# Optimization experiments

Hardware: AMD Instinct MI355X
Metric: run time of the kernel (lower is better)

Reference implementation:

```python
import jax, jax.numpy as jnp
import numpy as np

H = 40; W = 40; WS = 8; SHIFT = 4; NH = 10; C = 60; HD = C // NH
N = WS * WS; NW = (H // WS) * (W // WS); NB = 4; EPS = 1e-5

def _rel_pos_index():
    coords = np.stack(np.meshgrid(np.arange(WS), np.arange(WS), indexing='ij')).reshape(2, -1)
    rel = (coords[:, :, None] - coords[:, None, :]).transpose(1, 2, 0)
    rel[:, :, 0] += WS - 1; rel[:, :, 1] += WS - 1; rel[:, :, 0] *= 2 * WS - 1
    return jnp.asarray(rel.sum(-1))  # [N, N]

RPI = _rel_pos_index()

def _shift_mask():
    img = np.zeros((H, W))
    cnt = 0
    sls = (slice(0, -WS), slice(-WS, -SHIFT), slice(-SHIFT, None))
    for hs in sls:
        for ws_ in sls:
            img[hs, ws_] = cnt; cnt += 1
    mw = img.reshape(H // WS, WS, W // WS, WS).transpose(0, 2, 1, 3).reshape(NW, N)
    am = mw[:, None, :] - mw[:, :, None]
    return jnp.asarray(np.where(am != 0, -100.0, 0.0).astype(np.float32))  # [NW, N, N]

MASK = _shift_mask()

def _ln(x, g, b):
    m = x.mean(-1, keepdims=True)
    v = ((x - m) ** 2).mean(-1, keepdims=True)
    return (x - m) * jax.lax.rsqrt(v + EPS) * g + b

def _win_part(x):  # [B,H,W,C] -> [B*NW,N,C]
    B = x.shape[0]
    return x.reshape(B, H // WS, WS, W // WS, WS, C).transpose(0, 1, 3, 2, 4, 5).reshape(B * NW, N, C)

def _win_rev(x, B):  # [B*NW,N,C] -> [B,H,W,C]
    return x.reshape(B, H // WS, W // WS, WS, WS, C).transpose(0, 1, 3, 2, 4, 5).reshape(B, H, W, C)

def _block(x, p, shift):
    B = x.shape[0]
    g1, b1, qkvw, qkvb, rpb_t, pw, pb, g2, b2, f1w, f1b, f2w, f2b = p
    shortcut = x
    h = _ln(x, g1, b1).reshape(B, H, W, C)
    if shift:
        h = jnp.roll(h, (-shift, -shift), axis=(1, 2))
    xw = _win_part(h)                                   # [B*NW, N, C]
    qkv = (xw @ qkvw.T + qkvb).reshape(-1, N, 3, NH, HD).transpose(2, 0, 3, 1, 4)
    q, k, v = qkv[0], qkv[1], qkv[2]                    # [B*NW, NH, N, HD]
    attn = (q * (HD ** -0.5)) @ k.transpose(0, 1, 3, 2)  # [B*NW, NH, N, N]
    attn = attn + rpb_t[RPI].transpose(2, 0, 1)[None]
    if shift:
        attn = (attn.reshape(B, NW, NH, N, N) + MASK[None, :, None]).reshape(-1, NH, N, N)
    attn = jax.nn.softmax(attn, axis=-1)
    o = (attn @ v).transpose(0, 2, 1, 3).reshape(-1, N, C)
    o = o @ pw.T + pb
    h = _win_rev(o, B)
    if shift:
        h = jnp.roll(h, (shift, shift), axis=(1, 2))
    x = shortcut + h.reshape(B, H * W, C)
    y = _ln(x, g2, b2)
    y = jax.nn.gelu(y @ f1w.T + f1b, approximate=False) @ f2w.T + f2b
    return x + y

def _conv(x, w, b):
    y = jax.lax.conv_general_dilated(x, w, (1, 1), 'SAME', dimension_numbers=('NCHW', 'OIHW', 'NCHW'))
    return y + b[None, :, None, None]

def _forward(x, conv_in_w, conv_in_b, norm1_g, norm1_b, qkv_w, qkv_b, rpb, proj_w, proj_b,
             norm2_g, norm2_b, fc1_w, fc1_b, fc2_w, fc2_b, conv_out_w, conv_out_b):
    B = x.shape[0]
    h = _conv(x.reshape(B, -1, H, W), conv_in_w, conv_in_b)   # [B, C, H, W]
    h = h.reshape(B, C, H * W).transpose(0, 2, 1)             # [B, L, C]
    for i in range(NB):
        p = (norm1_g[i], norm1_b[i], qkv_w[i], qkv_b[i], rpb[i], proj_w[i], proj_b[i],
             norm2_g[i], norm2_b[i], fc1_w[i], fc1_b[i], fc2_w[i], fc2_b[i])
        h = _block(h, p, SHIFT if i % 2 == 1 else 0)
    h = h.transpose(0, 2, 1).reshape(B, C, H, W)
    return _conv(h, conv_out_w, conv_out_b)


def setup_inputs() -> dict:
    key = jax.random.key(0)
    ks = jax.random.split(key, 10)
    s = 0.02
    return {
        'x': jax.random.normal(ks[0], (128, 6, 3, H, W), jnp.float32),
        'conv_in_w': jax.random.normal(ks[1], (C, 18, 3, 3), jnp.float32) * s,
        'conv_in_b': jnp.zeros((C,), jnp.float32),
        'norm1_g': jnp.ones((NB, C), jnp.float32),
        'norm1_b': jnp.zeros((NB, C), jnp.float32),
        'qkv_w': jax.random.normal(ks[2], (NB, 3 * C, C), jnp.float32) * s,
        'qkv_b': jnp.zeros((NB, 3 * C), jnp.float32),
        'rpb': jax.random.normal(ks[3], (NB, (2 * WS - 1) ** 2, NH), jnp.float32) * s,
        'proj_w': jax.random.normal(ks[4], (NB, C, C), jnp.float32) * s,
        'proj_b': jnp.zeros((NB, C), jnp.float32),
        'norm2_g': jnp.ones((NB, C), jnp.float32),
        'norm2_b': jnp.zeros((NB, C), jnp.float32),
        'fc1_w': jax.random.normal(ks[5], (NB, 4 * C, C), jnp.float32) * s,
        'fc1_b': jnp.zeros((NB, 4 * C), jnp.float32),
        'fc2_w': jax.random.normal(ks[6], (NB, C, 4 * C), jnp.float32) * s,
        'fc2_b': jnp.zeros((NB, C), jnp.float32),
        'conv_out_w': jax.random.normal(ks[7], (3, C, 3, 3), jnp.float32) * s,
        'conv_out_b': jnp.zeros((3,), jnp.float32),
    }


def reference(x, conv_in_w, conv_in_b, norm1_g, norm1_b, qkv_w, qkv_b, rpb, proj_w, proj_b,
              norm2_g, norm2_b, fc1_w, fc1_b, fc2_w, fc2_b, conv_out_w, conv_out_b):
    return _forward(x, conv_in_w, conv_in_b, norm1_g, norm1_b, qkv_w, qkv_b, rpb, proj_w, proj_b,
                    norm2_g, norm2_b, fc1_w, fc1_b, fc2_w, fc2_b, conv_out_w, conv_out_b)
```

## Files before the change

### kernel.cpp

```cpp
#include <hip/hip_runtime.h>
#include <math.h>


typedef __bf16 bf16x8 __attribute__((ext_vector_type(8)));
typedef float f32x4 __attribute__((ext_vector_type(4)));
typedef unsigned int u32x4 __attribute__((ext_vector_type(4)));
typedef float f4u __attribute__((ext_vector_type(4), aligned(4)));

#define MFMA16(a, b, c) __builtin_amdgcn_mfma_f32_16x16x32_bf16(a, b, c, 0, 0, 0)

__device__ __forceinline__ unsigned short f2bf(float x) {
    unsigned u = __float_as_uint(x);
    return (unsigned short)((u + 0x7fffu + ((u >> 16) & 1u)) >> 16);
}
__device__ __forceinline__ unsigned short bfrn(float x) {
    return (unsigned short)((__float_as_uint(x) + 0x8000u) >> 16);
}
__device__ __forceinline__ unsigned pk2rn(float a, float b) {
    unsigned r;
    asm("v_cvt_pk_bf16_f32 %0, %1, %2" : "=v"(r) : "v"(a), "v"(b));
    return r;
}
__device__ __forceinline__ float bfsel(unsigned u, int hi) {
    return __uint_as_float(hi ? (u & 0xffff0000u) : (u << 16));
}
__device__ __forceinline__ float gelu_f(float v) {
    float t2 = v * v;
    float e = __builtin_amdgcn_exp2f(v * fmaf(0.102943225f, t2, 2.302207877f));
    float r = __builtin_amdgcn_rcpf(e + 1.f);
    return fmaf(-v, r, v);
}
__device__ __forceinline__ int gidx(int n, int wh, int wc, int shift) {
    int hh = wh * 8 + (n >> 3) + shift; if (hh >= 40) hh -= 40;
    int ww = wc * 8 + (n & 7) + shift;  if (ww >= 40) ww -= 40;
    return hh * 40 + ww;
}

__global__ __launch_bounds__(256) void prep_k(
    const float* __restrict__ qkvw, const float* __restrict__ pw,
    const float* __restrict__ f1w, const float* __restrict__ f2w,
    const float* __restrict__ qkvb, const float* __restrict__ pb,
    const float* __restrict__ f1b, const float* __restrict__ f2b,
    const float* __restrict__ g1v, const float* __restrict__ b1v,
    const float* __restrict__ g2v, const float* __restrict__ b2v,
    unsigned short* __restrict__ Wp)
{
    int t = blockIdx.x * 256 + threadIdx.x;
    int lane = t & 63;
    int q6 = t >> 6;
    int layer = q6 / 96, tile = q6 % 96;
    int l15 = lane & 15, l4 = lane >> 4;
    const float* src; const float* gam = 0; const float* bet = 0;
    float bias = 0.f, rowscale = 1.f;
    int row, stride, rmax, kmax, k0;
    unsigned short* dst = Wp + layer * 49152;
    if (tile < 24) {
        int ot = tile >> 1, ks = tile & 1;
        src = qkvw + layer * 10800; row = ot * 16 + l15; k0 = ks * 32 + l4 * 8;
        rmax = 180; kmax = 60; stride = 60; dst += tile * 512;
        gam = g1v + layer * 60; bet = b1v + layer * 60;
        if (row < 180) bias = qkvb[layer * 180 + row];
        if (row < 60) rowscale = 0.58897780f;
    } else if (tile < 32) {
        int tt = tile - 24;
        src = pw + layer * 3600; row = (tt >> 1) * 16 + l15; k0 = (tt & 1) * 32 + l4 * 8;
        rmax = 60; kmax = 60; stride = 60; dst += 12288 + tt * 512;
        if (row < 60) bias = pb[layer * 60 + row];
    } else if (tile < 64) {
        int tt = tile - 32; int ks = tt & 1; int po = tt >> 1; int ot = po & 7; int ph = po >> 3;
        src = f1w + layer * 14400 + ph * 7200; row = ot * 16 + l15; k0 = ks * 32 + l4 * 8;
        rmax = 120; kmax = 60; stride = 60; dst += 16384 + tt * 512;
        gam = g2v + layer * 60; bet = b2v + layer * 60;
        if (row < 120) bias = f1b[layer * 240 + ph * 120 + row];
    } else {
        int tt = tile - 64; int ks = tt & 3; int po = tt >> 2; int ot = po & 3; int ph = po >> 2;
        src = f2w + layer * 14400 + ph * 120; row = ot * 16 + l15; k0 = ks * 32 + l4 * 8;
        rmax = 60; kmax = 120; stride = 240; dst += 32768 + tt * 512;
        if (ph == 0 && row < 60) bias = f2b[layer * 60 + row];
    }
    unsigned short v[8];
    #pragma unroll
    for (int i = 0; i < 8; i++) {
        int k = k0 + i;
        float f = 0.f;
        if (row < rmax) {
            if (k < kmax) {
                f = src[row * stride + k];
                if (gam) f *= gam[k];
            } else if (k == kmax) {
                f = bias;
                if (bet) for (int kk = 0; kk < kmax; kk++) f += src[row * stride + kk] * bet[kk];
            }
        }
        v[i] = f2bf(f * rowscale);
    }
    unsigned a0 = (unsigned)v[0] | ((unsigned)v[1] << 16);
    unsigned a1 = (unsigned)v[2] | ((unsigned)v[3] << 16);
    unsigned a2 = (unsigned)v[4] | ((unsigned)v[5] << 16);
    unsigned a3 = (unsigned)v[6] | ((unsigned)v[7] << 16);
    *(uint4*)(dst + lane * 8) = make_uint4(a0, a1, a2, a3);
}

__global__ __launch_bounds__(256) void prepc_k(
    const float* __restrict__ ciw, const float* __restrict__ cow,
    unsigned short* __restrict__ Wc)
{
    int t = blockIdx.x * 256 + threadIdx.x;
    if (t >= 3456) return;
    int lane = t & 63, tile = t >> 6;
    int l15 = lane & 15, l4 = lane >> 4;
    unsigned short v[8];
    if (tile < 36) {
        int mt = tile / 9, g = tile % 9;
        int ky = g / 3, kx = g % 3;
        int row = mt * 16 + l15;
        int ci0 = l4 * 8;
        #pragma unroll
        for (int i = 0; i < 8; i++) {
            int ci = ci0 + i;
            float f = (row < 60 && ci < 18) ? ciw[(row * 18 + ci) * 9 + ky * 3 + kx] : 0.f;
            v[i] = f2bf(f);
        }
    } else {
        int tt = tile - 36;
        int g = tt >> 1, ks = tt & 1;
        int row = l15;
        int ci0 = ks * 32 + l4 * 8;
        #pragma unroll
        for (int i = 0; i < 8; i++) {
            int ci = ci0 + i;
            float f = (row < 3 && ci < 60) ? cow[(row * 60 + ci) * 9 + g] : 0.f;
            v[i] = f2bf(f);
        }
    }
    unsigned a0 = (unsigned)v[0] | ((unsigned)v[1] << 16);
    unsigned a1 = (unsigned)v[2] | ((unsigned)v[3] << 16);
    unsigned a2 = (unsigned)v[4] | ((unsigned)v[5] << 16);
    unsigned a3 = (unsigned)v[6] | ((unsigned)v[7] << 16);
    *(uint4*)(Wc + tile * 512 + lane * 8) = make_uint4(a0, a1, a2, a3);
}

__global__ __launch_bounds__(256) void rpbexp_k(
    const float* __restrict__ rpb, unsigned* __restrict__ rpbE)
{
    int layer = blockIdx.x / 5, hp = blockIdx.x % 5;
    int tid = threadIdx.x;
    int q = tid >> 2, j0 = (tid & 3) * 16;
    const float* rsrc = rpb + layer * 2250 + hp * 2;
    unsigned* dst = rpbE + ((layer * 5 + hp) * 64 + q) * 64 + j0;
    int qr = q >> 3, qc = q & 7;
    #pragma unroll
    for (int jj = 0; jj < 16; jj++) {
        int j = j0 + jj;
        int jr = j >> 3, jc = j & 7;
        int ridx = ((qr - jr + 7) * 15 + (qc - jc + 7)) * 10;
        unsigned short lo = f2bf(rsrc[ridx] * 1.4426950409f);
        unsigned short hi = f2bf(rsrc[ridx + 1] * 1.4426950409f);
        dst[jj] = (unsigned)lo | ((unsigned)hi << 16);
    }
}

__global__ __launch_bounds__(256) void conv_in_k(
    const float* __restrict__ x, const unsigned short* __restrict__ Wc,
    const float* __restrict__ bias, float* __restrict__ S)
{
    __shared__ __align__(16) unsigned short xt[10 * 42 * 32];
    int b = blockIdx.x / 5, y0 = (blockIdx.x % 5) * 8;
    int tid = threadIdx.x;
    int lane = tid & 63, w = tid >> 6;
    int l15 = lane & 15, l4 = lane >> 4;

    uint4* xt4 = (uint4*)xt;
    for (int i = tid; i < 1680; i += 256) xt4[i] = make_uint4(0u, 0u, 0u, 0u);
    __syncthreads();

    const float* xb = x + (size_t)b * 28800;
    for (int idx = tid; idx < 10 * 18 * 40; idx += 256) {
        int xx = idx % 40;
        int rem = idx / 40;
        int ci = rem % 18;
        int ry = rem / 18;
        int yy = y0 + ry - 1;
        if (yy >= 0 && yy < 40) {
            float v = xb[ci * 1600 + yy * 40 + xx];
            int xs = xx + 1;
            int bo = (((ry * 42 + xs) * 32 + ci) * 2) ^ ((xs & 3) << 4);
            *(unsigned short*)((char*)xt + bo) = bfrn(v);
        }
    }
    __syncthreads();

    bf16x8 afr[9];
    #pragma unroll
    for (int g = 0; g < 9; g++)
        afr[g] = *(const bf16x8*)(Wc + (w * 9 + g) * 512 + lane * 8);

    int c0 = w * 16 + l4 * 4;
    bool valid = (c0 < 60);
    f4u bv = {0.f, 0.f, 0.f, 0.f};
    if (valid) bv = *(const f4u*)(bias + c0);
    const f32x4 zf = {0.f, 0.f, 0.f, 0.f};
    const char* xtb = (const char*)xt;

    for (int nt = 0; nt < 20; nt++) {
        int tok = nt * 16 + l15;
        int yl = tok / 40, xl = tok % 40;
        f32x4 acc = zf;
        #pragma unroll
        for (int g = 0; g < 9; g++) {
            int ky = g / 3, kx = g % 3;
            int xs = xl + kx;
            int ba = ((yl + ky) * 42 + xs) * 64 + ((l4 ^ (xs & 3)) << 4);
            bf16x8 bfrag = *(const bf16x8*)(xtb + ba);
            acc = MFMA16(afr[g], bfrag, acc);
        }
        if (valid) {
            float4 r;
            r.x = acc[0] + bv[0]; r.y = acc[1] + bv[1];
            r.z = acc[2] + bv[2]; r.w = acc[3] + bv[3];
            *(float4*)(S + ((size_t)b * 1600 + y0 * 40 + tok) * 60 + c0) = r;
        }
    }
}

template<int SHIFT>
__global__ __launch_bounds__(256, 3) void block_k(
    float* __restrict__ S,
    const unsigned short* __restrict__ WpL,
    const unsigned* __restrict__ rpE)
{
    __shared__ __align__(16) unsigned char LDSA[53616];
    unsigned short* Pl  = (unsigned short*)(LDSA + 4608);
    float*          x1t = (float*)(LDSA + 0);
    unsigned short* xln = (unsigned short*)(LDSA + 15600);
    unsigned short* h1  = (unsigned short*)(LDSA + 15600);
    unsigned short* qn  = (unsigned short*)(LDSA + 24816);
    unsigned short* kn  = (unsigned short*)(LDSA + 34032);
    unsigned short* vt  = (unsigned short*)(LDSA + 43248);
    unsigned short* ln2 = (unsigned short*)(LDSA + 43248);

    const int tid = threadIdx.x;
    const int lane = tid & 63, w = tid >> 6;
    const int l15 = lane & 15, l4 = lane >> 4;
    const int wbase = w * 16;
    const int b = blockIdx.x / 25, wnd = blockIdx.x % 25;
    const int wh = wnd / 5, wc = wnd % 5;
    float* Sb = S + (size_t)b * 96000;
    const f32x4 zf = {0.f, 0.f, 0.f, 0.f};
    u32x4 zu = {0u, 0u, 0u, 0u};
    const bf16x8 zb = __builtin_bit_cast(bf16x8, zu);
    u32x4 ou = {0x3F803F80u, 0x3F803F80u, 0x3F803F80u, 0x3F803F80u};
    const bf16x8 ones = __builtin_bit_cast(bf16x8, ou);

    {
        int n = tid >> 2, p = tid & 3, cb = p * 16;
        int g = gidx(n, wh, wc, SHIFT);
        const float* xp = Sb + (size_t)g * 60 + cb;
        float xv[16];
        {
            float4 v0 = *(const float4*)xp;
            float4 v1 = *(const float4*)(xp + 4);
            float4 v2 = *(const float4*)(xp + 8);
            xv[0] = v0.x; xv[1] = v0.y; xv[2] = v0.z; xv[3] = v0.w;
            xv[4] = v1.x; xv[5] = v1.y; xv[6] = v1.z; xv[7] = v1.w;
            xv[8] = v2.x; xv[9] = v2.y; xv[10] = v2.z; xv[11] = v2.w;
            if (p < 3) {
                float4 v3 = *(const float4*)(xp + 12);
                xv[12] = v3.x; xv[13] = v3.y; xv[14] = v3.z; xv[15] = v3.w;
            } else { xv[12] = xv[13] = xv[14] = xv[15] = 0.f; }
        }
        float s = 0.f;
        #pragma unroll
        for (int ii = 0; ii < 16; ii++) s += xv[ii];
        s += __shfl_xor(s, 1); s += __shfl_xor(s, 2);
        float mean = s * (1.f / 60.f);
        float vv = 0.f;
        #pragma unroll
        for (int ii = 0; ii < 12; ii++) { float d = xv[ii] - mean; vv += d * d; }
        #pragma unroll
        for (int ii = 12; ii < 16; ii++) { float d = xv[ii] - mean; vv += (p < 3) ? d * d : 0.f; }
        vv += __shfl_xor(vv, 1); vv += __shfl_xor(vv, 2);
        float rs = rsqrtf(vv * (1.f / 60.f) + 1e-5f);
        float ov[16];
        #pragma unroll
        for (int ii = 0; ii < 12; ii++) ov[ii] = (xv[ii] - mean) * rs;
        #pragma unroll
        for (int ii = 12; ii < 16; ii++)
            ov[ii] = (p < 3) ? (xv[ii] - mean) * rs : ((ii == 12) ? 1.f : 0.f);
        unsigned short* xr = xln + n * 72 + cb;
        *(uint4*)xr = make_uint4(pk2rn(ov[0], ov[1]), pk2rn(ov[2], ov[3]),
                                 pk2rn(ov[4], ov[5]), pk2rn(ov[6], ov[7]));
        *(uint4*)(xr + 8) = make_uint4(pk2rn(ov[8], ov[9]), pk2rn(ov[10], ov[11]),
                                       pk2rn(ov[12], ov[13]), pk2rn(ov[14], ov[15]));
    }
    __syncthreads();

    {
        bf16x8 bx[4][2];
        #pragma unroll
        for (int nt = 0; nt < 4; nt++)
            #pragma unroll
            for (int ks = 0; ks < 2; ks++)
                bx[nt][ks] = *(const bf16x8*)(xln + (nt * 16 + l15) * 72 + l4 * 8 + ks * 32);
        #pragma unroll
        for (int t = 0; t < 3; t++) {
            int ot = w * 3 + t;
            f32x4 acc[4];
            #pragma unroll
            for (int nt = 0; nt < 4; nt++) acc[nt] = zf;
            #pragma unroll
            for (int ks = 0; ks < 2; ks++) {
                bf16x8 a = *(const bf16x8*)(WpL + (ot * 2 + ks) * 512 + lane * 8);
                #pragma unroll
                for (int nt = 0; nt < 4; nt++) acc[nt] = MFMA16(a, bx[nt][ks], acc[nt]);
            }
            int o0 = ot * 16 + l4 * 4;
            #pragma unroll
            for (int nt = 0; nt < 4; nt++) {
                int n = nt * 16 + l15;
                if (o0 < 60) {
                    *(uint2*)(qn + n * 72 + o0) =
                        make_uint2(pk2rn(acc[nt][0], acc[nt][1]), pk2rn(acc[nt][2], acc[nt][3]));
                } else if (o0 < 120) {
                    *(uint2*)(kn + n * 72 + (o0 - 60)) =
                        make_uint2(pk2rn(acc[nt][0], acc[nt][1]), pk2rn(acc[nt][2], acc[nt][3]));
                } else {
                    int r = o0 - 120;
                    vt[(r + 0) * 72 + n] = bfrn(acc[nt][0]);
                    vt[(r + 1) * 72 + n] = bfrn(acc[nt][1]);
                    vt[(r + 2) * 72 + n] = bfrn(acc[nt][2]);
                    vt[(r + 3) * 72 + n] = bfrn(acc[nt][3]);
                }
            }
        }
    }
    __syncthreads();

    unsigned maskbits = 0u;
    if (SHIFT) {
        int qtok = wbase + l15;
        int qr = qtok >> 3, qc = qtok & 7;
        int shp = wh * 8 + qr, swp = wc * 8 + qc;
        int qreg = (shp < 32 ? 0 : (shp < 36 ? 1 : 2)) * 3 + (swp < 32 ? 0 : (swp < 36 ? 1 : 2));
        #pragma unroll
        for (int e = 0; e < 16; e++) {
            int jt = e >> 2, r = e & 3;
            int j = jt * 16 + l4 * 4 + r;
            int jr = j >> 3, jc = j & 7;
            int shq = wh * 8 + jr, swq = wc * 8 + jc;
            int jreg = (shq < 32 ? 0 : (shq < 36 ? 1 : 2)) * 3 + (swq < 32 ? 0 : (swq < 36 ? 1 : 2));
            if (jreg != qreg) maskbits |= (1u << e);
        }
    }

    f32x4 oacc[10];
    #pragma unroll
    for (int h = 0; h < 10; h++) oacc[h] = zf;
    unsigned short* prow = Pl + (wbase + l15) * 72;
    const unsigned* rpq = rpE + ((wbase + l15) << 6) + (l4 << 2);

    u32x4 rpc[4];
    #pragma unroll
    for (int jt = 0; jt < 4; jt++) rpc[jt] = *(const u32x4*)(rpq + jt * 16);

    #pragma unroll
    for (int hp = 0; hp < 5; hp++) {
        u32x4 rpn[4];
        if (hp < 4) {
            const unsigned* rq = rpq + (hp + 1) * 4096;
            #pragma unroll
            for (int jt = 0; jt < 4; jt++) rpn[jt] = *(const u32x4*)(rq + jt * 16);
        }
        #pragma unroll
        for (int hh2 = 0; hh2 < 2; hh2++) {
            const int h = hp * 2 + hh2;
            bf16x8 bq = zb, ak0 = zb, ak1 = zb, ak2 = zb, ak3 = zb;
            if (l4 == 0) {
                const unsigned* qp = (const unsigned*)(qn + (wbase + l15) * 72 + h * 6);
                u32x4 uq = {qp[0], qp[1], qp[2], 0u};
                bq = __builtin_bit_cast(bf16x8, uq);
                const unsigned* k0p = (const unsigned*)(kn + (0 * 16 + l15) * 72 + h * 6);
                const unsigned* k1p = (const unsigned*)(kn + (1 * 16 + l15) * 72 + h * 6);
                const unsigned* k2p = (const unsigned*)(kn + (2 * 16 + l15) * 72 + h * 6);
                const unsigned* k3p = (const unsigned*)(kn + (3 * 16 + l15) * 72 + h * 6);
                u32x4 u0 = {k0p[0], k0p[1], k0p[2], 0u}; ak0 = __builtin_bit_cast(bf16x8, u0);
                u32x4 u1 = {k1p[0], k1p[1], k1p[2], 0u}; ak1 = __builtin_bit_cast(bf16x8, u1);
                u32x4 u2 = {k2p[0], k2p[1], k2p[2], 0u}; ak2 = __builtin_bit_cast(bf16x8, u2);
                u32x4 u3 = {k3p[0], k3p[1], k3p[2], 0u}; ak3 = __builtin_bit_cast(bf16x8, u3);
            }
            f32x4 s0 = MFMA16(ak0, bq, zf);
            f32x4 s1 = MFMA16(ak1, bq, zf);
            f32x4 s2 = MFMA16(ak2, bq, zf);
            f32x4 s3 = MFMA16(ak3, bq, zf);
            float ee[16];
            #pragma unroll
            for (int r = 0; r < 4; r++) {
                ee[0 + r]  = __builtin_amdgcn_exp2f(s0[r] + bfsel(rpc[0][r], hh2));
                ee[4 + r]  = __builtin_amdgcn_exp2f(s1[r] + bfsel(rpc[1][r], hh2));
                ee[8 + r]  = __builtin_amdgcn_exp2f(s2[r] + bfsel(rpc[2][r], hh2));
                ee[12 + r] = __builtin_amdgcn_exp2f(s3[r] + bfsel(rpc[3][r], hh2));
            }
            if (SHIFT) {
                #pragma unroll
                for (int e = 0; e < 16; e++)
                    if (maskbits & (1u << e)) ee[e] = 0.f;
            }
            #pragma unroll
            for (int jt = 0; jt < 4; jt++)
                *(uint2*)(prow + jt * 16 + l4 * 4) =
                    make_uint2(pk2rn(ee[jt * 4 + 0], ee[jt * 4 + 1]),
                               pk2rn(ee[jt * 4 + 2], ee[jt * 4 + 3]));
            asm volatile("s_waitcnt lgkmcnt(0)" ::: "memory");
            bf16x8 ap0 = *(const bf16x8*)(prow + l4 * 8);
            bf16x8 ap1 = *(const bf16x8*)(prow + 32 + l4 * 8);
            bf16x8 bv0 = *(const bf16x8*)(vt + (h * 6 + l15) * 72 + l4 * 8);
            bf16x8 bv1 = *(const bf16x8*)(vt + (h * 6 + l15) * 72 + 32 + l4 * 8);
            f32x4 sm = MFMA16(ap0, ones, zf);
            sm = MFMA16(ap1, ones, sm);
            f32x4 pv = MFMA16(ap0, bv0, zf);
            pv = MFMA16(ap1, bv1, pv);
            #pragma unroll
            for (int r = 0; r < 4; r++)
                oacc[h][r] = pv[r] * __builtin_amdgcn_rcpf(sm[r]);
        }
        #pragma unroll
        for (int jt = 0; jt < 4; jt++) rpc[jt] = rpn[jt];
    }

    unsigned short* olds = qn;
    if (l15 < 6) {
        #pragma unroll
        for (int h = 0; h < 10; h++)
            #pragma unroll
            for (int j = 0; j < 4; j++)
                olds[(wbase + l4 * 4 + j) * 72 + h * 6 + l15] = bfrn(oacc[h][j]);
    } else if (l15 < 10) {
        unsigned short pv16 = (l15 == 6) ? (unsigned short)0x3F80 : (unsigned short)0;
        #pragma unroll
        for (int j = 0; j < 4; j++)
            olds[(wbase + l4 * 4 + j) * 72 + 60 + (l15 - 6)] = pv16;
    }
    __syncthreads();

    {
        bf16x8 bo0 = *(const bf16x8*)(olds + (wbase + l15) * 72 + l4 * 8);
        bf16x8 bo1 = *(const bf16x8*)(olds + (wbase + l15) * 72 + 32 + l4 * 8);
        f32x4 acc[4];
        #pragma unroll
        for (int ot = 0; ot < 4; ot++) acc[ot] = zf;
        #pragma unroll
        for (int ot = 0; ot < 4; ot++) {
            bf16x8 a0 = *(const bf16x8*)(WpL + 12288 + (ot * 2 + 0) * 512 + lane * 8);
            bf16x8 a1 = *(const bf16x8*)(WpL + 12288 + (ot * 2 + 1) * 512 + lane * 8);
            acc[ot] = MFMA16(a0, bo0, acc[ot]);
            acc[ot] = MFMA16(a1, bo1, acc[ot]);
        }
        int n = wbase + l15;
        int g = gidx(n, wh, wc, SHIFT);
        #pragma unroll
        for (int ot = 0; ot < 4; ot++) {
            int o0 = ot * 16 + l4 * 4;
            if (o0 < 60) {
                float4 xr = *(const float4*)(Sb + (size_t)g * 60 + o0);
                x1t[(o0 + 0) * 65 + n] = xr.x + acc[ot][0];
                x1t[(o0 + 1) * 65 + n] = xr.y + acc[ot][1];
                x1t[(o0 + 2) * 65 + n] = xr.z + acc[ot][2];
                x1t[(o0 + 3) * 65 + n] = xr.w + acc[ot][3];
            }
        }
    }
    asm volatile("s_waitcnt lgkmcnt(0)" ::: "memory");

    {
        int n = wbase + (lane >> 2), p = lane & 3, cb = p * 16;
        float xv[16];
        #pragma unroll
        for (int ii = 0; ii < 12; ii++) xv[ii] = x1t[(cb + ii) * 65 + n];
        #pragma unroll
        for (int ii = 12; ii < 16; ii++) xv[ii] = (p < 3) ? x1t[(cb + ii) * 65 + n] : 0.f;
        float s = 0.f;
        #pragma unroll
        for (int ii = 0; ii < 16; ii++) s += xv[ii];
        s += __shfl_xor(s, 1); s += __shfl_xor(s, 2);
        float mean = s * (1.f / 60.f);
        float vv = 0.f;
        #pragma unroll
        for (int ii = 0; ii < 12; ii++) { float d = xv[ii] - mean; vv += d * d; }
        #pragma unroll
        for (int ii = 12; ii < 16; ii++) { float d = xv[ii] - mean; vv += (p < 3) ? d * d : 0.f; }
        vv += __shfl_xor(vv, 1); vv += __shfl_xor(vv, 2);
        float rs = rsqrtf(vv * (1.f / 60.f) + 1e-5f);
        float ov[16];
        #pragma unroll
        for (int ii = 0; ii < 12; ii++) ov[ii] = (xv[ii] - mean) * rs;
        #pragma unroll
        for (int ii = 12; ii < 16; ii++)
            ov[ii] = (p < 3) ? (xv[ii] - mean) * rs : ((ii == 12) ? 1.f : 0.f);
        unsigned short* lr = ln2 + n * 72 + cb;
        *(uint4*)lr = make_uint4(pk2rn(ov[0], ov[1]), pk2rn(ov[2], ov[3]),
                                 pk2rn(ov[4], ov[5]), pk2rn(ov[6], ov[7]));
        *(uint4*)(lr + 8) = make_uint4(pk2rn(ov[8], ov[9]), pk2rn(ov[10], ov[11]),
                                       pk2rn(ov[12], ov[13]), pk2rn(ov[14], ov[15]));
    }
    __syncthreads();

    f32x4 acc2[4];
    #pragma unroll
    for (int ot = 0; ot < 4; ot++) acc2[ot] = zf;

    #pragma unroll
    for (int ph = 0; ph < 2; ph++) {
        {
            bf16x8 bl[4][2];
            #pragma unroll
            for (int nt = 0; nt < 4; nt++)
                #pragma unroll
                for (int ks = 0; ks < 2; ks++)
                    bl[nt][ks] = *(const bf16x8*)(ln2 + (nt * 16 + l15) * 72 + l4 * 8 + ks * 32);
            #pragma unroll
            for (int t = 0; t < 2; t++) {
                int ot = w + t * 4;
                f32x4 a1[4];
                #pragma unroll
                for (int nt = 0; nt < 4; nt++) a1[nt] = zf;
                #pragma unroll
                for (int ks = 0; ks < 2; ks++) {
                    bf16x8 a = *(const bf16x8*)(WpL + 16384 + ((ph * 8 + ot) * 2 + ks) * 512 + lane * 8);
                    #pragma unroll
                    for (int nt = 0; nt < 4; nt++) a1[nt] = MFMA16(a, bl[nt][ks], a1[nt]);
                }
                int o0 = ot * 16 + l4 * 4;
                if (o0 < 120) {
                    #pragma unroll
                    for (int nt = 0; nt < 4; nt++) {
                        int n = nt * 16 + l15;
                        *(uint2*)(h1 + n * 136 + o0) =
                            make_uint2(pk2rn(gelu_f(a1[nt][0]), gelu_f(a1[nt][1])),
                                       pk2rn(gelu_f(a1[nt][2]), gelu_f(a1[nt][3])));
                    }
                }
            }
            if (ph == 0 && tid < 64)
                *(uint4*)(h1 + tid * 136 + 120) = make_uint4(0x3F80u, 0u, 0u, 0u);
        }
        __syncthreads();
        {
            bf16x8 bh[4];
            #pragma unroll
            for (int ks = 0; ks < 4; ks++)
                bh[ks] = *(const bf16x8*)(h1 + (wbase + l15) * 136 + l4 * 8 + ks * 32);
            #pragma unroll
            for (int ot = 0; ot < 4; ot++)
                #pragma unroll
                for (int ks = 0; ks < 4; ks++) {
                    bf16x8 a = *(const bf16x8*)(WpL + 32768 + ((ph * 4 + ot) * 4 + ks) * 512 + lane * 8);
                    acc2[ot] = MFMA16(a, bh[ks], acc2[ot]);
                }
        }
        if (ph == 0) __syncthreads();
    }

    {
        int n = wbase + l15;
        int g = gidx(n, wh, wc, SHIFT);
        #pragma unroll
        for (int ot = 0; ot < 4; ot++) {
            int o0 = ot * 16 + l4 * 4;
            if (o0 < 60) {
                float4 r;
                r.x = x1t[(o0 + 0) * 65 + n] + acc2[ot][0];
                r.y = x1t[(o0 + 1) * 65 + n] + acc2[ot][1];
                r.z = x1t[(o0 + 2) * 65 + n] + acc2[ot][2];
                r.w = x1t[(o0 + 3) * 65 + n] + acc2[ot][3];
                *(float4*)(Sb + (size_t)g * 60 + o0) = r;
            }
        }
    }
}

__global__ __launch_bounds__(256) void conv_out_k(
    const float* __restrict__ S, const unsigned short* __restrict__ Wc2,
    const float* __restrict__ bias, float* __restrict__ out)
{
    __shared__ __align__(16) unsigned short st[6 * 42 * 64];
    int b = blockIdx.x / 10, y0 = (blockIdx.x % 10) * 4;
    int tid = threadIdx.x;
    int lane = tid & 63, w = tid >> 6;
    int l15 = lane & 15, l4 = lane >> 4;

    uint4* st4 = (uint4*)st;
    for (int i = tid; i < 2016; i += 256) st4[i] = make_uint4(0u, 0u, 0u, 0u);
    __syncthreads();

    const float* Sb = S + (size_t)b * 96000;
    for (int idx = tid; idx < 3600; idx += 256) {
        int cg = idx % 15;
        int xx = (idx / 15) % 40;
        int ry = idx / 600;
        int yy = y0 + ry - 1;
        if (yy >= 0 && yy < 40) {
            const float* sp = Sb + ((size_t)yy * 40 + xx) * 60 + cg * 4;
            float4 v = *(const float4*)sp;
            int xs = xx + 1;
            int bo = (ry * 42 + xs) * 128 + ((cg * 8) ^ ((xs & 7) << 4));
            *(uint2*)((char*)st + bo) = make_uint2(pk2rn(v.x, v.y), pk2rn(v.z, v.w));
        }
    }
    __syncthreads();

    bf16x8 afr[9][2];
    #pragma unroll
    for (int g = 0; g < 9; g++)
        #pragma unroll
        for (int ks = 0; ks < 2; ks++)
            afr[g][ks] = *(const bf16x8*)(Wc2 + (g * 2 + ks) * 512 + lane * 8);

    float b0 = bias[0], b1 = bias[1], b2 = bias[2];
    const f32x4 zf = {0.f, 0.f, 0.f, 0.f};
    const char* stb = (const char*)st;

    for (int nt = w; nt < 10; nt += 4) {
        int tok = nt * 16 + l15;
        int yl = tok / 40, xl = tok % 40;
        f32x4 acc = zf;
        #pragma unroll
        for (int g = 0; g < 9; g++) {
            int ky = g / 3, kx = g % 3;
            int xs = xl + kx;
            int base = ((yl + ky) * 42 + xs) * 128;
            #pragma unroll
            for (int ks = 0; ks < 2; ks++) {
                int bo = base + (((ks * 4 + l4) ^ (xs & 7)) << 4);
                bf16x8 bfrag = *(const bf16x8*)(stb + bo);
                acc = MFMA16(afr[g][ks], bfrag, acc);
            }
        }
        if (l4 == 0) {
            int y = y0 + yl;
            float* op = out + (size_t)b * 4800 + y * 40 + xl;
            op[0] = acc[0] + b0;
            op[1600] = acc[1] + b1;
            op[3200] = acc[2] + b2;
        }
    }
}

extern "C" void kernel_launch(void* const* d_in, const int* in_sizes, int n_in,
                              void* d_out, int out_size, void* d_ws, size_t ws_size,
                              hipStream_t stream)
{
    const float* x   = (const float*)d_in[0];
    const float* ciw = (const float*)d_in[1];
    const float* cib = (const float*)d_in[2];
    const float* n1g = (const float*)d_in[3];
    const float* n1b = (const float*)d_in[4];
    const float* qw  = (const float*)d_in[5];
    const float* qb  = (const float*)d_in[6];
    const float* rpb = (const float*)d_in[7];
    const float* pw  = (const float*)d_in[8];
    const float* pb  = (const float*)d_in[9];
    const float* n2g = (const float*)d_in[10];
    const float* n2b = (const float*)d_in[11];
    const float* f1w = (const float*)d_in[12];
    const float* f1b = (const float*)d_in[13];
    const float* f2w = (const float*)d_in[14];
    const float* f2b = (const float*)d_in[15];
    const float* cow = (const float*)d_in[16];
    const float* cob = (const float*)d_in[17];
    float* out = (float*)d_out;
    float* S = (float*)d_ws;
    unsigned short* Wp = (unsigned short*)((char*)d_ws + 49152000);
    unsigned* rpbE = (unsigned*)((char*)d_ws + 49545216);
    unsigned short* Wc = (unsigned short*)((char*)d_ws + 49872896);

    prep_k<<<96, 256, 0, stream>>>(qw, pw, f1w, f2w, qb, pb, f1b, f2b,
                                   n1g, n1b, n2g, n2b, Wp);
    prepc_k<<<14, 256, 0, stream>>>(ciw, cow, Wc);
    rpbexp_k<<<20, 256, 0, stream>>>(rpb, rpbE);
    conv_in_k<<<128 * 5, 256, 0, stream>>>(x, Wc, cib, S);
    for (int i = 0; i < 4; i++) {
        const unsigned short* WpL = Wp + i * 49152;
        const unsigned* rpEL = rpbE + i * 5 * 4096;
        if (i & 1) block_k<4><<<128 * 25, 256, 0, stream>>>(S, WpL, rpEL);
        else       block_k<0><<<128 * 25, 256, 0, stream>>>(S, WpL, rpEL);
    }
    conv_out_k<<<128 * 10, 256, 0, stream>>>(S, Wc + 36 * 512, cob, out);
}
```

Before: 417.6 us.

## Keep post-attention residual in registers and shrink LDS for higher occupancy

```diff
diff --git a/kernel.cpp b/kernel.cpp
--- a/kernel.cpp
+++ b/kernel.cpp
@@ -224,20 +224,19 @@
 }
 
 template<int SHIFT>
-__global__ __launch_bounds__(256, 3) void block_k(
+__global__ __launch_bounds__(256, 4) void block_k(
     float* __restrict__ S,
     const unsigned short* __restrict__ WpL,
     const unsigned* __restrict__ rpE)
 {
-    __shared__ __align__(16) unsigned char LDSA[53616];
-    unsigned short* Pl  = (unsigned short*)(LDSA + 4608);
-    float*          x1t = (float*)(LDSA + 0);
-    unsigned short* xln = (unsigned short*)(LDSA + 15600);
-    unsigned short* h1  = (unsigned short*)(LDSA + 15600);
-    unsigned short* qn  = (unsigned short*)(LDSA + 24816);
-    unsigned short* kn  = (unsigned short*)(LDSA + 34032);
-    unsigned short* vt  = (unsigned short*)(LDSA + 43248);
-    unsigned short* ln2 = (unsigned short*)(LDSA + 43248);
+    __shared__ __align__(16) unsigned char LDSA[38016];
+    unsigned short* xln = (unsigned short*)(LDSA + 0);
+    unsigned short* Pl  = (unsigned short*)(LDSA + 0);
+    unsigned short* h1  = (unsigned short*)(LDSA + 0);
+    unsigned short* qn  = (unsigned short*)(LDSA + 9216);
+    unsigned short* kn  = (unsigned short*)(LDSA + 18432);
+    unsigned short* vt  = (unsigned short*)(LDSA + 27648);
+    unsigned short* ln2 = (unsigned short*)(LDSA + 27648);
 
     const int tid = threadIdx.x;
     const int lane = tid & 63, w = tid >> 6;
@@ -442,6 +441,7 @@
     }
     __syncthreads();
 
+    f32x4 x1v[4];
     {
         bf16x8 bo0 = *(const bf16x8*)(olds + (wbase + l15) * 72 + l4 * 8);
         bf16x8 bo1 = *(const bf16x8*)(olds + (wbase + l15) * 72 + 32 + l4 * 8);
@@ -462,45 +462,47 @@
             int o0 = ot * 16 + l4 * 4;
             if (o0 < 60) {
                 float4 xr = *(const float4*)(Sb + (size_t)g * 60 + o0);
-                x1t[(o0 + 0) * 65 + n] = xr.x + acc[ot][0];
-                x1t[(o0 + 1) * 65 + n] = xr.y + acc[ot][1];
-                x1t[(o0 + 2) * 65 + n] = xr.z + acc[ot][2];
-                x1t[(o0 + 3) * 65 + n] = xr.w + acc[ot][3];
-            }
-        }
-    }
-    asm volatile("s_waitcnt lgkmcnt(0)" ::: "memory");
+                x1v[ot][0] = xr.x + acc[ot][0];
+                x1v[ot][1] = xr.y + acc[ot][1];
+                x1v[ot][2] = xr.z + acc[ot][2];
+                x1v[ot][3] = xr.w + acc[ot][3];
+            } else {
+                x1v[ot] = zf;
+            }
+        }
+    }
 
     {
-        int n = wbase + (lane >> 2), p = lane & 3, cb = p * 16;
-        float xv[16];
-        #pragma unroll
-        for (int ii = 0; ii < 12; ii++) xv[ii] = x1t[(cb + ii) * 65 + n];
-        #pragma unroll
-        for (int ii = 12; ii < 16; ii++) xv[ii] = (p < 3) ? x1t[(cb + ii) * 65 + n] : 0.f;
         float s = 0.f;
         #pragma unroll
-        for (int ii = 0; ii < 16; ii++) s += xv[ii];
-        s += __shfl_xor(s, 1); s += __shfl_xor(s, 2);
+        for (int ot = 0; ot < 4; ot++)
+            #pragma unroll
+            for (int r = 0; r < 4; r++) s += x1v[ot][r];
+        s += __shfl_xor(s, 16); s += __shfl_xor(s, 32);
         float mean = s * (1.f / 60.f);
         float vv = 0.f;
         #pragma unroll
-        for (int ii = 0; ii < 12; ii++) { float d = xv[ii] - mean; vv += d * d; }
-        #pragma unroll
-        for (int ii = 12; ii < 16; ii++) { float d = xv[ii] - mean; vv += (p < 3) ? d * d : 0.f; }
-        vv += __shfl_xor(vv, 1); vv += __shfl_xor(vv, 2);
+        for (int ot = 0; ot < 4; ot++) {
+            int o0 = ot * 16 + l4 * 4;
+            if (o0 < 60) {
+                #pragma unroll
+                for (int r = 0; r < 4; r++) { float d = x1v[ot][r] - mean; vv += d * d; }
+            }
+        }
+        vv += __shfl_xor(vv, 16); vv += __shfl_xor(vv, 32);
         float rs = rsqrtf(vv * (1.f / 60.f) + 1e-5f);
-        float ov[16];
-        #pragma unroll
-        for (int ii = 0; ii < 12; ii++) ov[ii] = (xv[ii] - mean) * rs;
-        #pragma unroll
-        for (int ii = 12; ii < 16; ii++)
-            ov[ii] = (p < 3) ? (xv[ii] - mean) * rs : ((ii == 12) ? 1.f : 0.f);
-        unsigned short* lr = ln2 + n * 72 + cb;
-        *(uint4*)lr = make_uint4(pk2rn(ov[0], ov[1]), pk2rn(ov[2], ov[3]),
-                                 pk2rn(ov[4], ov[5]), pk2rn(ov[6], ov[7]));
-        *(uint4*)(lr + 8) = make_uint4(pk2rn(ov[8], ov[9]), pk2rn(ov[10], ov[11]),
-                                       pk2rn(ov[12], ov[13]), pk2rn(ov[14], ov[15]));
+        int n = wbase + l15;
+        #pragma unroll
+        for (int ot = 0; ot < 4; ot++) {
+            int o0 = ot * 16 + l4 * 4;
+            if (o0 < 60) {
+                *(uint2*)(ln2 + n * 72 + o0) = make_uint2(
+                    pk2rn((x1v[ot][0] - mean) * rs, (x1v[ot][1] - mean) * rs),
+                    pk2rn((x1v[ot][2] - mean) * rs, (x1v[ot][3] - mean) * rs));
+            } else {
+                *(uint2*)(ln2 + n * 72 + 60) = make_uint2(0x00003F80u, 0u);
+            }
+        }
     }
     __syncthreads();
 
@@ -568,10 +570,10 @@
             int o0 = ot * 16 + l4 * 4;
             if (o0 < 60) {
                 float4 r;
-                r.x = x1t[(o0 + 0) * 65 + n] + acc2[ot][0];
-                r.y = x1t[(o0 + 1) * 65 + n] + acc2[ot][1];
-                r.z = x1t[(o0 + 2) * 65 + n] + acc2[ot][2];
-                r.w = x1t[(o0 + 3) * 65 + n] + acc2[ot][3];
+                r.x = x1v[ot][0] + acc2[ot][0];
+                r.y = x1v[ot][1] + acc2[ot][1];
+                r.z = x1v[ot][2] + acc2[ot][2];
+                r.w = x1v[ot][3] + acc2[ot][3];
                 *(float4*)(Sb + (size_t)g * 60 + o0) = r;
             }
         }
```

After: 393.8 us. 1.06x faster.
